# Kernel tuning notes

Hardware: AMD Instinct MI355X
Metric: run time of the kernel (lower is better)

The kernel has to match this reference:

```python
import jax, jax.numpy as jnp
import numpy as np

MIN_DIST = 0.1
BIG = 1e10

def setup_inputs() -> dict:
    key = jax.random.key(0)
    kV, kP, kN, kF, kE = jax.random.split(key, 5)
    B, N, F, P = 4, 8192, 8192, 2048
    mesh_V = jax.random.normal(kV, (B, N, 3), dtype=jnp.float32)
    points = jax.random.normal(kP, (B, P, 3), dtype=jnp.float32)
    fn = jax.random.normal(kN, (B, F, 3), dtype=jnp.float32)
    mesh_FN = fn / jnp.linalg.norm(fn, axis=-1, keepdims=True)  # unit face normals
    mesh_F = jax.random.randint(kF, (B, F, 3), 0, N, dtype=jnp.int32)
    exterior_flag = jax.random.bernoulli(kE, 0.5, (B, P, 1))
    return {"mesh_V": mesh_V, "points": points, "mesh_FN": mesh_FN,
            "mesh_F": mesh_F, "exterior_flag": exterior_flag}

def reference(mesh_V, points, mesh_FN, mesh_F, exterior_flag):
    B, P, _ = points.shape
    fn = jax.lax.stop_gradient(mesh_FN)                       # normals are detached
    # gather face vertices: (B,F,3verts,3)
    face_points = jax.vmap(lambda V, Fi: V[Fi])(mesh_V, mesh_F)
    face_center = jnp.mean(face_points, axis=-2)              # (B,F,3)
    # signed distance of each point to each face plane
    diff = points[:, :, None, :] - face_center[:, None, :, :] # (B,P,F,3)
    signed = jnp.sum(diff * fn[:, None, :, :], axis=-1) + MIN_DIST  # (B,P,F)
    # ||signed * n||^2 = signed^2 * ||n||^2  (avoids (B,P,F,3) re-materialization)
    fn_sq = jnp.sum(fn * fn, axis=-1)                         # (B,F)
    sqdist = (signed * signed) * fn_sq[:, None, :]            # (B,P,F)
    sqdist = jnp.where(signed < 0, BIG, sqdist)
    min_sqdist = jnp.min(sqdist, axis=-1)                     # (B,P)
    inside = (~exterior_flag.reshape(B, P)) | jnp.all(signed < 0, axis=-1)
    min_sqdist = jnp.where(inside, 0.0, min_sqdist)
    per_batch = jnp.mean(min_sqdist, axis=1)                  # reduction='mean'
    return jnp.mean(per_batch, axis=0)                        # scalar
```

## Files before the change

kernel.cpp:

```cpp
#include <hip/hip_runtime.h>
#include <math.h>

#define Bn 4
#define Nn 8192
#define Fn 8192
#define Pn 2048
#define NCHUNK 128
#define CH (Fn / NCHUNK)
#define MIN_DIST 0.1f

__global__ __launch_bounds__(256)
void face_pre(const float* __restrict__ V, const float* __restrict__ FN,
              const int* __restrict__ Fidx, float4* __restrict__ fd) {
    int i = blockIdx.x * 256 + threadIdx.x;
    if (i >= Bn * Fn) return;
    int b = i / Fn;
    const int* fi = Fidx + (size_t)i * 3;
    int i0 = fi[0], i1 = fi[1], i2 = fi[2];
    const float* Vb = V + (size_t)b * Nn * 3;
    float cx = (Vb[i0*3+0] + Vb[i1*3+0] + Vb[i2*3+0]) / 3.0f;
    float cy = (Vb[i0*3+1] + Vb[i1*3+1] + Vb[i2*3+1]) / 3.0f;
    float cz = (Vb[i0*3+2] + Vb[i1*3+2] + Vb[i2*3+2]) / 3.0f;
    const float* n = FN + (size_t)i * 3;
    float nx = n[0], ny = n[1], nz = n[2];
    float d = MIN_DIST - (cx*nx + cy*ny + cz*nz);
    float s = sqrtf(nx*nx + ny*ny + nz*nz);
    fd[i] = make_float4(nx*s, ny*s, nz*s, d*s);
}

__global__ void detect_mode(const unsigned char* __restrict__ flags, int* __restrict__ mode) {
    __shared__ int cnt;
    if (threadIdx.x == 0) cnt = 0;
    __syncthreads();
    int local = 0;
    for (int i = threadIdx.x; i < Bn * Pn; i += 256)
        if ((i & 3) && flags[i]) local++;
    if (local) atomicAdd(&cnt, local);
    __syncthreads();
    if (threadIdx.x == 0) *mode = (cnt > 0) ? 1 : 0;
}

__global__ __launch_bounds__(256)
void chunk_min(const float* __restrict__ points, const float4* __restrict__ fd,
               unsigned* __restrict__ partials) {
    int c = blockIdx.x % NCHUNK;
    int b = blockIdx.x / NCHUNK;
    int tid = threadIdx.x;

    __shared__ float4 lf[CH];
    ((float*)lf)[tid] = ((const float*)(fd + (size_t)b * Fn + (size_t)c * CH))[tid];

    float px[8], py[8], pz[8];
    const float* pb = points + (size_t)b * Pn * 3;
#pragma unroll
    for (int k = 0; k < 8; ++k) {
        int p = tid + 256 * k;
        px[k] = pb[p*3+0]; py[k] = pb[p*3+1]; pz[k] = pb[p*3+2];
    }
    unsigned m[8];
#pragma unroll
    for (int k = 0; k < 8; ++k) m[k] = 0x7F7FFFFFu;

    __syncthreads();

#pragma unroll 4
    for (int j = 0; j < CH; ++j) {
        float4 f = lf[j];
#pragma unroll
        for (int k = 0; k < 8; ++k) {
            float s = fmaf(px[k], f.x, fmaf(py[k], f.y, fmaf(pz[k], f.z, f.w)));
            unsigned su = __float_as_uint(s);
            m[k] = su < m[k] ? su : m[k];
        }
    }

    unsigned* out = partials + (size_t)c * (Bn * Pn) + (size_t)b * Pn;
#pragma unroll
    for (int k = 0; k < 8; ++k) out[tid + 256 * k] = m[k];
}

__global__ __launch_bounds__(256)
void point_reduce(const unsigned* __restrict__ partials,
                  const unsigned char* __restrict__ flagsB,
                  const int* __restrict__ flagsI,
                  const int* __restrict__ mode,
                  float* __restrict__ blocksums) {
    int i = blockIdx.x * 256 + threadIdx.x;
    unsigned m = 0x7F7FFFFFu;
    for (int c = 0; c < NCHUNK; ++c) {
        unsigned v = partials[(size_t)c * (Bn * Pn) + i];
        m = v < m ? v : m;
    }
    float mf = __uint_as_float(m);
    int ext = (*mode) ? (flagsB[i] != 0) : (flagsI[i] != 0);
    float val = (ext && mf < 1e9f) ? mf * mf : 0.0f;

    for (int o = 32; o > 0; o >>= 1) val += __shfl_down(val, o);
    __shared__ float wsum[4];
    int lane = threadIdx.x & 63, wid = threadIdx.x >> 6;
    if (lane == 0) wsum[wid] = val;
    __syncthreads();
    if (threadIdx.x == 0)
        blocksums[blockIdx.x] = wsum[0] + wsum[1] + wsum[2] + wsum[3];
}

__global__ void finalize(const float* __restrict__ blocksums, float* __restrict__ out) {
    float v = (threadIdx.x < (Bn * Pn) / 256) ? blocksums[threadIdx.x] : 0.0f;
    for (int o = 32; o > 0; o >>= 1) v += __shfl_down(v, o);
    if (threadIdx.x == 0) out[0] = v * (1.0f / (Bn * Pn));
}

extern "C" void kernel_launch(void* const* d_in, const int* in_sizes, int n_in,
                              void* d_out, int out_size, void* d_ws, size_t ws_size,
                              hipStream_t stream) {
    const float* mesh_V  = (const float*)d_in[0];
    const float* points  = (const float*)d_in[1];
    const float* mesh_FN = (const float*)d_in[2];
    const int*   mesh_F  = (const int*)d_in[3];
    const void*  eflag   = d_in[4];
    float* out = (float*)d_out;

    char* ws = (char*)d_ws;
    const size_t faceBytes = (size_t)Bn * Fn * sizeof(float4);
    const size_t partBytes = (size_t)NCHUNK * Bn * Pn * sizeof(unsigned);
    float4*   faceData  = (float4*)ws;
    unsigned* partials  = (unsigned*)(ws + faceBytes);
    float*    blocksums = (float*)(ws + faceBytes + partBytes);
    int*      mode      = (int*)(ws + faceBytes + partBytes + 256);

    face_pre<<<(Bn * Fn + 255) / 256, 256, 0, stream>>>(mesh_V, mesh_FN, mesh_F, faceData);
    detect_mode<<<1, 256, 0, stream>>>((const unsigned char*)eflag, mode);
    chunk_min<<<Bn * NCHUNK, 256, 0, stream>>>(points, faceData, partials);
    point_reduce<<<(Bn * Pn) / 256, 256, 0, stream>>>(partials,
                                                      (const unsigned char*)eflag,
                                                      (const int*)eflag, mode, blocksums);
    finalize<<<1, 64, 0, stream>>>(blocksums, out);
}
```

Before: 91.02 us.

## Fuse face precompute, mode detection and finalize into chunk and reduce kernels

Face plane precomputation moves into chunk_min, with each block building its own 32-face chunk in shared memory, and flag-mode detection moves into block 0 of that kernel. The final sum uses an atomic ticket in point_reduce in place of a separate finalize kernel. Together this cuts the launch count from five to two. NCHUNK doubles to 256, giving 1024 blocks, and the inner loop uses packed 2-wide float FMAs. The risks are a longer reduction over 256 partials per point, a non-deterministic float atomic sum, and extra serial work in block 0.

```diff
diff --git a/kernel.cpp b/kernel.cpp
--- a/kernel.cpp
+++ b/kernel.cpp
@@ -5,109 +5,136 @@
 #define Nn 8192
 #define Fn 8192
 #define Pn 2048
-#define NCHUNK 128
+#define NCHUNK 256
 #define CH (Fn / NCHUNK)
+#define PPT 8
 #define MIN_DIST 0.1f
+#define FLTMAX_BITS 0x7F7FFFFFu
+
+typedef float v2f __attribute__((ext_vector_type(2)));
+
+struct Meta { float acc; int cnt; int mode; };
 
 __global__ __launch_bounds__(256)
-void face_pre(const float* __restrict__ V, const float* __restrict__ FN,
-              const int* __restrict__ Fidx, float4* __restrict__ fd) {
-    int i = blockIdx.x * 256 + threadIdx.x;
-    if (i >= Bn * Fn) return;
-    int b = i / Fn;
-    const int* fi = Fidx + (size_t)i * 3;
-    int i0 = fi[0], i1 = fi[1], i2 = fi[2];
-    const float* Vb = V + (size_t)b * Nn * 3;
-    float cx = (Vb[i0*3+0] + Vb[i1*3+0] + Vb[i2*3+0]) / 3.0f;
-    float cy = (Vb[i0*3+1] + Vb[i1*3+1] + Vb[i2*3+1]) / 3.0f;
-    float cz = (Vb[i0*3+2] + Vb[i1*3+2] + Vb[i2*3+2]) / 3.0f;
-    const float* n = FN + (size_t)i * 3;
-    float nx = n[0], ny = n[1], nz = n[2];
-    float d = MIN_DIST - (cx*nx + cy*ny + cz*nz);
-    float s = sqrtf(nx*nx + ny*ny + nz*nz);
-    fd[i] = make_float4(nx*s, ny*s, nz*s, d*s);
-}
-
-__global__ void detect_mode(const unsigned char* __restrict__ flags, int* __restrict__ mode) {
-    __shared__ int cnt;
-    if (threadIdx.x == 0) cnt = 0;
-    __syncthreads();
-    int local = 0;
-    for (int i = threadIdx.x; i < Bn * Pn; i += 256)
-        if ((i & 3) && flags[i]) local++;
-    if (local) atomicAdd(&cnt, local);
-    __syncthreads();
-    if (threadIdx.x == 0) *mode = (cnt > 0) ? 1 : 0;
-}
-
-__global__ __launch_bounds__(256)
-void chunk_min(const float* __restrict__ points, const float4* __restrict__ fd,
-               unsigned* __restrict__ partials) {
-    int c = blockIdx.x % NCHUNK;
-    int b = blockIdx.x / NCHUNK;
+void chunk_min(const float* __restrict__ V, const float* __restrict__ FN,
+               const int* __restrict__ Fidx, const float* __restrict__ points,
+               const unsigned char* __restrict__ flags,
+               unsigned* __restrict__ partials, Meta* __restrict__ meta) {
+    int c = blockIdx.x & (NCHUNK - 1);
+    int b = blockIdx.x >> 8;
     int tid = threadIdx.x;
 
     __shared__ float4 lf[CH];
-    ((float*)lf)[tid] = ((const float*)(fd + (size_t)b * Fn + (size_t)c * CH))[tid];
 
-    float px[8], py[8], pz[8];
+    if (tid < CH) {
+        int i = b * Fn + c * CH + tid;
+        const int* fi = Fidx + (size_t)i * 3;
+        int i0 = fi[0], i1 = fi[1], i2 = fi[2];
+        const float* Vb = V + (size_t)b * Nn * 3;
+        float cx = (Vb[i0*3+0] + Vb[i1*3+0] + Vb[i2*3+0]) * (1.0f/3.0f);
+        float cy = (Vb[i0*3+1] + Vb[i1*3+1] + Vb[i2*3+1]) * (1.0f/3.0f);
+        float cz = (Vb[i0*3+2] + Vb[i1*3+2] + Vb[i2*3+2]) * (1.0f/3.0f);
+        const float* n = FN + (size_t)i * 3;
+        float nx = n[0], ny = n[1], nz = n[2];
+        float d = MIN_DIST - (cx*nx + cy*ny + cz*nz);
+        float s = sqrtf(nx*nx + ny*ny + nz*nz);
+        lf[tid] = make_float4(nx*s, ny*s, nz*s, d*s);
+    }
+
+    v2f px[PPT/2], py[PPT/2], pz[PPT/2];
     const float* pb = points + (size_t)b * Pn * 3;
 #pragma unroll
-    for (int k = 0; k < 8; ++k) {
-        int p = tid + 256 * k;
-        px[k] = pb[p*3+0]; py[k] = pb[p*3+1]; pz[k] = pb[p*3+2];
+    for (int k = 0; k < PPT/2; ++k) {
+        int p0 = tid + 256 * (2*k);
+        int p1 = p0 + 256;
+        px[k] = (v2f){pb[p0*3+0], pb[p1*3+0]};
+        py[k] = (v2f){pb[p0*3+1], pb[p1*3+1]};
+        pz[k] = (v2f){pb[p0*3+2], pb[p1*3+2]};
     }
-    unsigned m[8];
+    unsigned m[PPT];
 #pragma unroll
-    for (int k = 0; k < 8; ++k) m[k] = 0x7F7FFFFFu;
+    for (int k = 0; k < PPT; ++k) m[k] = FLTMAX_BITS;
 
     __syncthreads();
 
 #pragma unroll 4
     for (int j = 0; j < CH; ++j) {
         float4 f = lf[j];
+        v2f fx = (v2f){f.x, f.x}, fy = (v2f){f.y, f.y},
+            fz = (v2f){f.z, f.z}, fw = (v2f){f.w, f.w};
 #pragma unroll
-        for (int k = 0; k < 8; ++k) {
-            float s = fmaf(px[k], f.x, fmaf(py[k], f.y, fmaf(pz[k], f.z, f.w)));
-            unsigned su = __float_as_uint(s);
-            m[k] = su < m[k] ? su : m[k];
+        for (int k = 0; k < PPT/2; ++k) {
+#if __has_builtin(__builtin_elementwise_fma)
+            v2f s = __builtin_elementwise_fma(px[k], fx,
+                    __builtin_elementwise_fma(py[k], fy,
+                    __builtin_elementwise_fma(pz[k], fz, fw)));
+#else
+            v2f s;
+            s.x = fmaf(px[k].x, f.x, fmaf(py[k].x, f.y, fmaf(pz[k].x, f.z, f.w)));
+            s.y = fmaf(px[k].y, f.x, fmaf(py[k].y, f.y, fmaf(pz[k].y, f.z, f.w)));
+#endif
+            unsigned sx = __float_as_uint(s.x);
+            unsigned sy = __float_as_uint(s.y);
+            m[2*k]   = sx < m[2*k]   ? sx : m[2*k];
+            m[2*k+1] = sy < m[2*k+1] ? sy : m[2*k+1];
         }
     }
 
     unsigned* out = partials + (size_t)c * (Bn * Pn) + (size_t)b * Pn;
 #pragma unroll
-    for (int k = 0; k < 8; ++k) out[tid + 256 * k] = m[k];
+    for (int k = 0; k < PPT/2; ++k) {
+        out[tid + 256 * (2*k)]     = m[2*k];
+        out[tid + 256 * (2*k) + 256] = m[2*k+1];
+    }
+
+    if (blockIdx.x == 0) {
+        __shared__ int cnt;
+        if (tid == 0) cnt = 0;
+        __syncthreads();
+        int local = 0;
+        for (int i = tid; i < Bn * Pn; i += 256)
+            if ((i & 3) && flags[i]) local++;
+        if (local) atomicAdd(&cnt, local);
+        __syncthreads();
+        if (tid == 0) {
+            meta->mode = (cnt > 0) ? 1 : 0;
+            meta->acc = 0.0f;
+            meta->cnt = 0;
+        }
+    }
 }
 
 __global__ __launch_bounds__(256)
 void point_reduce(const unsigned* __restrict__ partials,
                   const unsigned char* __restrict__ flagsB,
                   const int* __restrict__ flagsI,
-                  const int* __restrict__ mode,
-                  float* __restrict__ blocksums) {
+                  Meta* __restrict__ meta, float* __restrict__ out) {
     int i = blockIdx.x * 256 + threadIdx.x;
-    unsigned m = 0x7F7FFFFFu;
+    unsigned m = FLTMAX_BITS;
+#pragma unroll 8
     for (int c = 0; c < NCHUNK; ++c) {
         unsigned v = partials[(size_t)c * (Bn * Pn) + i];
         m = v < m ? v : m;
     }
+    int ext = (meta->mode) ? (flagsB[i] != 0) : (flagsI[i] != 0);
     float mf = __uint_as_float(m);
-    int ext = (*mode) ? (flagsB[i] != 0) : (flagsI[i] != 0);
-    float val = (ext && mf < 1e9f) ? mf * mf : 0.0f;
+    float val = (ext && m < FLTMAX_BITS) ? mf * mf : 0.0f;
 
     for (int o = 32; o > 0; o >>= 1) val += __shfl_down(val, o);
     __shared__ float wsum[4];
     int lane = threadIdx.x & 63, wid = threadIdx.x >> 6;
     if (lane == 0) wsum[wid] = val;
     __syncthreads();
-    if (threadIdx.x == 0)
-        blocksums[blockIdx.x] = wsum[0] + wsum[1] + wsum[2] + wsum[3];
-}
-
-__global__ void finalize(const float* __restrict__ blocksums, float* __restrict__ out) {
-    float v = (threadIdx.x < (Bn * Pn) / 256) ? blocksums[threadIdx.x] : 0.0f;
-    for (int o = 32; o > 0; o >>= 1) v += __shfl_down(v, o);
-    if (threadIdx.x == 0) out[0] = v * (1.0f / (Bn * Pn));
+    if (threadIdx.x == 0) {
+        float s = wsum[0] + wsum[1] + wsum[2] + wsum[3];
+        atomicAdd(&meta->acc, s);
+        __threadfence();
+        int ticket = atomicAdd(&meta->cnt, 1);
+        if (ticket == gridDim.x - 1) {
+            float total = atomicAdd(&meta->acc, 0.0f);
+            out[0] = total * (1.0f / (Bn * Pn));
+        }
+    }
 }
 
 extern "C" void kernel_launch(void* const* d_in, const int* in_sizes, int n_in,
@@ -121,18 +148,14 @@
     float* out = (float*)d_out;
 
     char* ws = (char*)d_ws;
-    const size_t faceBytes = (size_t)Bn * Fn * sizeof(float4);
     const size_t partBytes = (size_t)NCHUNK * Bn * Pn * sizeof(unsigned);
-    float4*   faceData  = (float4*)ws;
-    unsigned* partials  = (unsigned*)(ws + faceBytes);
-    float*    blocksums = (float*)(ws + faceBytes + partBytes);
-    int*      mode      = (int*)(ws + faceBytes + partBytes + 256);
+    unsigned* partials = (unsigned*)ws;
+    Meta*     meta     = (Meta*)(ws + partBytes);
 
-    face_pre<<<(Bn * Fn + 255) / 256, 256, 0, stream>>>(mesh_V, mesh_FN, mesh_F, faceData);
-    detect_mode<<<1, 256, 0, stream>>>((const unsigned char*)eflag, mode);
-    chunk_min<<<Bn * NCHUNK, 256, 0, stream>>>(points, faceData, partials);
+    chunk_min<<<Bn * NCHUNK, 256, 0, stream>>>(mesh_V, mesh_FN, mesh_F, points,
+                                               (const unsigned char*)eflag,
+                                               partials, meta);
     point_reduce<<<(Bn * Pn) / 256, 256, 0, stream>>>(partials,
                                                       (const unsigned char*)eflag,
-                                                      (const int*)eflag, mode, blocksums);
-    finalize<<<1, 64, 0, stream>>>(blocksums, out);
+                                                      (const int*)eflag, meta, out);
 }
```

New measurement: 86.51 us. -5.0%, faster.
